# Kernel optimization log

Measured on AMD Instinct MI355X. Metric: run time of the kernel, lower is better.

Reference implementation:

```python
import jax, jax.numpy as jnp
import numpy as np

N = 50000
E = 800000
F_IN = 256
C = 64  # embedding_size, heads=1
EDGE_DIM = 2
NEG_SLOPE = 0.01


def setup_inputs() -> dict:
    key = jax.random.key(0)
    ks = jax.random.split(key, 12)
    s = 1.0 / np.sqrt(C)
    return {
        "x": jax.random.normal(ks[0], (N, F_IN), jnp.float32),
        "edge_index": jax.random.randint(ks[1], (2, E), 0, N, jnp.int64),
        "edge_attr": jax.random.normal(ks[2], (E, EDGE_DIM), jnp.float32),
        "Wf": jax.random.normal(ks[3], (F_IN, C), jnp.float32) / np.sqrt(F_IN),
        "bf": jnp.zeros((C,), jnp.float32),
        "Wq": jax.random.normal(ks[4], (C, C), jnp.float32) * s,
        "bq": jnp.zeros((C,), jnp.float32),
        "Wk": jax.random.normal(ks[5], (C, C), jnp.float32) * s,
        "bk": jnp.zeros((C,), jnp.float32),
        "Wv": jax.random.normal(ks[6], (C, C), jnp.float32) * s,
        "bv": jnp.zeros((C,), jnp.float32),
        "We": jax.random.normal(ks[7], (EDGE_DIM, C), jnp.float32) / np.sqrt(EDGE_DIM),
        "Wskip": jax.random.normal(ks[8], (C, C), jnp.float32) * s,
        "bskip": jnp.zeros((C,), jnp.float32),
    }


def reference(x, edge_index, edge_attr, Wf, bf, Wq, bq, Wk, bk, Wv, bv, We, Wskip, bskip):
    n = x.shape[0]
    src, dst = edge_index[0], edge_index[1]
    inv_sqrt_c = 1.0 / np.sqrt(C)

    h = jax.nn.leaky_relu(x @ Wf + bf, NEG_SLOPE)
    e = edge_attr @ We  # [E, C] edge embedding (lin_edge, no bias), same each layer

    for _ in range(3):
        q = h @ Wq + bq
        k = h @ Wk + bk
        v = h @ Wv + bv
        kj = k[src] + e                                  # [E, C] key + edge feat
        alpha = jnp.sum(q[dst] * kj, axis=-1) * inv_sqrt_c  # [E]
        # per-destination softmax
        m = jax.ops.segment_max(alpha, dst, num_segments=n)
        ex = jnp.exp(alpha - m[dst])
        den = jax.ops.segment_sum(ex, dst, num_segments=n)
        a = ex / den[dst]                                # [E]
        msg = (v[src] + e) * a[:, None]                  # [E, C]
        agg = jax.ops.segment_sum(msg, dst, num_segments=n)  # [N, C]
        h = jax.nn.leaky_relu(agg + h @ Wskip + bskip, NEG_SLOPE)  # root_weight skip
    return h
```

## Files before the change

### kernel.cpp

```cpp
#include <hip/hip_runtime.h>
#include <hip/hip_fp16.h>

#define NN 50000
#define NE 800000
#define FIN 256
#define C 64
#define NEG_SLOPE 0.01f
#define SCAN_BLOCKS ((NN + 255) / 256)
#define CSR_CHUNKS (NE / 256)

typedef float f32x16 __attribute__((ext_vector_type(16)));

__device__ __forceinline__ float leaky(float v) { return v > 0.f ? v : NEG_SLOPE * v; }

__global__ __launch_bounds__(256) void k_tw(const float* __restrict__ Wq,
                                            const float* __restrict__ Wk,
                                            const float* __restrict__ Wv,
                                            const float* __restrict__ Ws,
                                            float* __restrict__ Wt) {
    const int idx = blockIdx.x * 256 + threadIdx.x;
    if (idx >= 4 * 64 * 64) return;
    const int m = idx >> 12, r = idx & 4095, c = r >> 6, k = r & 63;
    const float* W = (m == 0) ? Wq : (m == 1) ? Wk : (m == 2) ? Wv : Ws;
    Wt[idx] = W[k * 64 + c];
}

#define FEAT_NPB 16

__global__ __launch_bounds__(256) void k_feat(const float* __restrict__ x,
                                              const float* __restrict__ Wf,
                                              const float* __restrict__ bf,
                                              float* __restrict__ h) {
    __shared__ float4 Sx[FEAT_NPB][64];
    __shared__ float part[FEAT_NPB][4][64];
    const int t = threadIdx.x;
    const int lane = t & 63;
    const int w = __builtin_amdgcn_readfirstlane(t) >> 6;
    const int base = blockIdx.x * FEAT_NPB;

    const float4* x4 = (const float4*)x;
#pragma unroll
    for (int i = 0; i < 4; ++i) {
        const int idx = t + i * 256;
        const int row = idx >> 6, c4 = idx & 63;
        Sx[row][c4] = x4[(size_t)(base + row) * 64 + c4];
    }

    float wrk[64];
#pragma unroll
    for (int k = 0; k < 64; ++k)
        wrk[k] = Wf[(size_t)(w * 64 + k) * 64 + lane];

    __syncthreads();

#pragma unroll
    for (int i = 0; i < FEAT_NPB; ++i) {
        float a0 = 0.f, a1 = 0.f, a2 = 0.f, a3 = 0.f;
#pragma unroll
        for (int j = 0; j < 16; ++j) {
            const float4 xv = Sx[i][w * 16 + j];
            a0 = fmaf(xv.x, wrk[4 * j + 0], a0);
            a1 = fmaf(xv.y, wrk[4 * j + 1], a1);
            a2 = fmaf(xv.z, wrk[4 * j + 2], a2);
            a3 = fmaf(xv.w, wrk[4 * j + 3], a3);
        }
        part[i][w][lane] = (a0 + a1) + (a2 + a3);
    }
    __syncthreads();

#pragma unroll
    for (int j = 0; j < 4; ++j) {
        const int o = t + j * 256;
        const int node = o >> 6, col = o & 63;
        const float r = part[node][0][col] + part[node][1][col]
                      + part[node][2][col] + part[node][3][col] + bf[col];
        h[(size_t)(base + node) * 64 + col] = leaky(r);
    }
}

#define QKVS_NPB 32

__global__ __launch_bounds__(256) void k_qkvs(const float* __restrict__ h,
                                              const float* __restrict__ Wt,
                                              const float* __restrict__ bq,
                                              const float* __restrict__ bk,
                                              const float* __restrict__ bv,
                                              const float* __restrict__ bs,
                                              float* __restrict__ qkvs) {
    const int t = threadIdx.x;
    const int lane = t & 63;
    const int sec = __builtin_amdgcn_readfirstlane(t) >> 6;
    const int base = blockIdx.x * QKVS_NPB;

    int m, cidx;
    float bias;
    if (sec == 0)      { m = 0; cidx = lane; bias = bq[lane]; }
    else if (sec == 1) { m = 3; cidx = lane; bias = bs[lane]; }
    else {
        cidx = ((sec - 2) << 5) + (lane >> 1);
        m = 1 + (lane & 1);
        bias = (lane & 1) ? bv[cidx] : bk[cidx];
    }

    const float4* wb = (const float4*)(Wt + ((size_t)m << 12) + ((size_t)cidx << 6));
    float4 w[16];
#pragma unroll
    for (int j = 0; j < 16; ++j) w[j] = wb[j];

    const int nmax = (base + QKVS_NPB <= NN) ? QKVS_NPB : (NN - base);
    for (int i = 0; i < nmax; ++i) {
        const float* hrow = h + (size_t)(base + i) * 64;
        f32x16 ha, hb, hc, hd;
        asm volatile("s_load_dwordx16 %0, %4, 0x0\n\t"
                     "s_load_dwordx16 %1, %4, 0x40\n\t"
                     "s_load_dwordx16 %2, %4, 0x80\n\t"
                     "s_load_dwordx16 %3, %4, 0xc0\n\t"
                     "s_waitcnt lgkmcnt(0)"
                     : "=&s"(ha), "=&s"(hb), "=&s"(hc), "=&s"(hd)
                     : "s"(hrow));
        float a0 = 0.f, a1 = 0.f, a2 = 0.f, a3 = 0.f;
#pragma unroll
        for (int j = 0; j < 4; ++j) {
            a0 = fmaf(ha[4 * j + 0], w[j].x, a0);
            a1 = fmaf(ha[4 * j + 1], w[j].y, a1);
            a2 = fmaf(ha[4 * j + 2], w[j].z, a2);
            a3 = fmaf(ha[4 * j + 3], w[j].w, a3);
        }
#pragma unroll
        for (int j = 0; j < 4; ++j) {
            a0 = fmaf(hb[4 * j + 0], w[4 + j].x, a0);
            a1 = fmaf(hb[4 * j + 1], w[4 + j].y, a1);
            a2 = fmaf(hb[4 * j + 2], w[4 + j].z, a2);
            a3 = fmaf(hb[4 * j + 3], w[4 + j].w, a3);
        }
#pragma unroll
        for (int j = 0; j < 4; ++j) {
            a0 = fmaf(hc[4 * j + 0], w[8 + j].x, a0);
            a1 = fmaf(hc[4 * j + 1], w[8 + j].y, a1);
            a2 = fmaf(hc[4 * j + 2], w[8 + j].z, a2);
            a3 = fmaf(hc[4 * j + 3], w[8 + j].w, a3);
        }
#pragma unroll
        for (int j = 0; j < 4; ++j) {
            a0 = fmaf(hd[4 * j + 0], w[12 + j].x, a0);
            a1 = fmaf(hd[4 * j + 1], w[12 + j].y, a1);
            a2 = fmaf(hd[4 * j + 2], w[12 + j].z, a2);
            a3 = fmaf(hd[4 * j + 3], w[12 + j].w, a3);
        }
        const float val = ((a0 + a1) + (a2 + a3)) + bias;
        float* orow = qkvs + (size_t)(base + i) * 192;
        if (sec == 0) {
            orow[lane] = val;
        } else if (sec == 1) {
            orow[128 + lane] = val;
        } else {
            __half* kvh = (__half*)(orow + 64);
            kvh[((sec - 2) << 6) + lane] = __float2half(val);
        }
    }
}

__global__ __launch_bounds__(256) void k_hist(const int* __restrict__ ei,
                                              int* __restrict__ deg) {
    const int e = blockIdx.x * 256 + threadIdx.x;
    if (e >= NE) return;
    atomicAdd(&deg[ei[NE + e]], 1);
}

__global__ __launch_bounds__(256) void k_blocksum(const int* __restrict__ deg,
                                                  int* __restrict__ bsum) {
    __shared__ int sh[256];
    const int t = threadIdx.x;
    const int idx = blockIdx.x * 256 + t;
    sh[t] = (idx < NN) ? deg[idx] : 0;
    __syncthreads();
#pragma unroll
    for (int off = 128; off > 0; off >>= 1) {
        if (t < off) sh[t] += sh[t + off];
        __syncthreads();
    }
    if (t == 0) bsum[blockIdx.x] = sh[0];
}

__global__ __launch_bounds__(256) void k_scanb(const int* __restrict__ bsum,
                                               int* __restrict__ boff) {
    __shared__ int sh[256];
    const int t = threadIdx.x;
    const int v = (t < SCAN_BLOCKS) ? bsum[t] : 0;
    sh[t] = v;
    __syncthreads();
#pragma unroll
    for (int off = 1; off < 256; off <<= 1) {
        const int x = (t >= off) ? sh[t - off] : 0;
        __syncthreads();
        sh[t] += x;
        __syncthreads();
    }
    if (t < SCAN_BLOCKS) boff[t] = sh[t] - v;
}

__global__ __launch_bounds__(256) void k_writeptr(const int* __restrict__ deg,
                                                  const int* __restrict__ boff,
                                                  int* __restrict__ row_ptr,
                                                  int* __restrict__ cursor) {
    __shared__ int sh[256];
    const int t = threadIdx.x;
    const int idx = blockIdx.x * 256 + t;
    const int v = (idx < NN) ? deg[idx] : 0;
    sh[t] = v;
    __syncthreads();
#pragma unroll
    for (int off = 1; off < 256; off <<= 1) {
        const int x = (t >= off) ? sh[t - off] : 0;
        __syncthreads();
        sh[t] += x;
        __syncthreads();
    }
    if (idx < NN) {
        const int r = boff[blockIdx.x] + sh[t] - v;
        row_ptr[idx] = r;
        cursor[idx] = r;
    }
    if (idx == 0) row_ptr[NN] = NE;
}

__global__ __launch_bounds__(256) void k_csr(const int* __restrict__ ei,
                                             const float* __restrict__ eattr,
                                             const int* __restrict__ row_ptr,
                                             int* __restrict__ cursor,
                                             uint2* __restrict__ erec) {
    const int chunk = blockIdx.x >> 3;
    const unsigned myx = blockIdx.x & 7;
    const int e = chunk * 256 + threadIdx.x;
    const int dst = ei[NE + e];
    const int rp = row_ptr[dst];
    const unsigned owner = (unsigned)rp / (NE / 8u);
    if (owner != myx) return;
    const int pos = atomicAdd(&cursor[dst], 1);
    const __half2 a = __floats2half2_rn(eattr[e * 2], eattr[e * 2 + 1]);
    erec[pos] = make_uint2((unsigned)ei[e], *(const unsigned*)&a);
}

__global__ __launch_bounds__(256) void k_conv(const int* __restrict__ row_ptr,
                                              const uint2* __restrict__ erec,
                                              const float* __restrict__ We,
                                              const float* __restrict__ qkvs,
                                              float* __restrict__ hout) {
    const int t = threadIdx.x;
    const int lane = t & 63;
    const int g = lane >> 4;
    const int p = lane & 15;
    const int wv = __builtin_amdgcn_readfirstlane(t) >> 6;
    const int d = blockIdx.x * 4 + wv;
    if (d >= NN) return;

    const float* qrow = qkvs + (size_t)d * 192;
    const float4 q4  = *(const float4*)(qrow + 4 * p);
    const float4 w0  = *(const float4*)(We + 4 * p);
    const float4 w1  = *(const float4*)(We + 64 + 4 * p);

    float pg0 = q4.x * w0.x + q4.y * w0.y + q4.z * w0.z + q4.w * w0.w;
    float pg1 = q4.x * w1.x + q4.y * w1.y + q4.z * w1.z + q4.w * w1.w;
#pragma unroll
    for (int mask = 1; mask <= 8; mask <<= 1) {
        pg0 += __shfl_xor(pg0, mask);
        pg1 += __shfl_xor(pg1, mask);
    }
    const float g0 = pg0, g1 = pg1;

    const int i0 = row_ptr[d], i1 = row_ptr[d + 1];
    const char* kvbase = (const char*)qkvs + 256 + ((size_t)p << 4);

    float m = -1e30f, l = 0.f, S1 = 0.f, S2 = 0.f;
    float4 acc = make_float4(0.f, 0.f, 0.f, 0.f);

#pragma unroll 2
    for (int i = i0 + g; i < i1; i += 4) {
        const uint2 r = erec[i];
        const __half2 ah = *(const __half2*)&r.y;
        const float a0 = __low2float(ah), a1 = __high2float(ah);
        const float4 kvl = *(const float4*)(kvbase + (size_t)r.x * 768);
        const __half2* hv = (const __half2*)&kvl;
        const float kf0 = __low2float(hv[0]), vf0 = __high2float(hv[0]);
        const float kf1 = __low2float(hv[1]), vf1 = __high2float(hv[1]);
        const float kf2 = __low2float(hv[2]), vf2 = __high2float(hv[2]);
        const float kf3 = __low2float(hv[3]), vf3 = __high2float(hv[3]);
        float dot = q4.x * kf0 + q4.y * kf1 + q4.z * kf2 + q4.w * kf3;
        dot += __shfl_xor(dot, 1);
        dot += __shfl_xor(dot, 2);
        dot += __shfl_xor(dot, 4);
        dot += __shfl_xor(dot, 8);
        const float P = (dot + g0 * a0 + g1 * a1) * 0.125f;
        const float mn = fmaxf(m, P);
        const float s = __expf(m - mn);
        const float e = __expf(P - mn);
        l = l * s + e;
        acc.x = acc.x * s + vf0 * e;
        acc.y = acc.y * s + vf1 * e;
        acc.z = acc.z * s + vf2 * e;
        acc.w = acc.w * s + vf3 * e;
        S1 = S1 * s + a0 * e;
        S2 = S2 * s + a1 * e;
        m = mn;
    }

#pragma unroll
    for (int mask = 16; mask <= 32; mask <<= 1) {
        const float mo  = __shfl_xor(m, mask);
        const float lo  = __shfl_xor(l, mask);
        const float axo = __shfl_xor(acc.x, mask);
        const float ayo = __shfl_xor(acc.y, mask);
        const float azo = __shfl_xor(acc.z, mask);
        const float awo = __shfl_xor(acc.w, mask);
        const float S1o = __shfl_xor(S1, mask);
        const float S2o = __shfl_xor(S2, mask);
        const float mn = fmaxf(m, mo);
        const float sA = __expf(m - mn);
        const float sB = __expf(mo - mn);
        l     = l * sA + lo * sB;
        acc.x = acc.x * sA + axo * sB;
        acc.y = acc.y * sA + ayo * sB;
        acc.z = acc.z * sA + azo * sB;
        acc.w = acc.w * sA + awo * sB;
        S1    = S1 * sA + S1o * sB;
        S2    = S2 * sA + S2o * sB;
        m = mn;
    }

    if (lane < 16) {
        const float inv = (l > 0.f) ? 1.f / l : 0.f;
        const float4 sk = *(const float4*)(qrow + 128 + 4 * p);
        float4 r;
        r.x = leaky((acc.x + S1 * w0.x + S2 * w1.x) * inv + sk.x);
        r.y = leaky((acc.y + S1 * w0.y + S2 * w1.y) * inv + sk.y);
        r.z = leaky((acc.z + S1 * w0.z + S2 * w1.z) * inv + sk.z);
        r.w = leaky((acc.w + S1 * w0.w + S2 * w1.w) * inv + sk.w);
        *(float4*)(hout + (size_t)d * C + 4 * p) = r;
    }
}

extern "C" void kernel_launch(void* const* d_in, const int* in_sizes, int n_in,
                              void* d_out, int out_size, void* d_ws, size_t ws_size,
                              hipStream_t stream) {
    const float* x     = (const float*)d_in[0];
    const int*   ei    = (const int*)d_in[1];
    const float* eattr = (const float*)d_in[2];
    const float* Wf    = (const float*)d_in[3];
    const float* bf    = (const float*)d_in[4];
    const float* Wq    = (const float*)d_in[5];
    const float* bq    = (const float*)d_in[6];
    const float* Wk    = (const float*)d_in[7];
    const float* bk    = (const float*)d_in[8];
    const float* Wv    = (const float*)d_in[9];
    const float* bv    = (const float*)d_in[10];
    const float* We    = (const float*)d_in[11];
    const float* Ws    = (const float*)d_in[12];
    const float* bs    = (const float*)d_in[13];
    float* out = (float*)d_out;

    char* p = (char*)d_ws;
    float*  h       = (float*)p;  p += (size_t)NN * C * 4;
    float*  qkvs    = (float*)p;  p += (size_t)NN * 192 * 4;
    float*  Wt      = (float*)p;  p += (size_t)4 * 64 * 64 * 4;
    int*    deg     = (int*)p;    p += (size_t)NN * 4;
    int*    row_ptr = (int*)p;    p += (size_t)(NN + 1) * 4;
    int*    cursor  = (int*)p;    p += (size_t)NN * 4;
    int*    bsum    = (int*)p;    p += (size_t)SCAN_BLOCKS * 4;
    int*    boff    = (int*)p;    p += (size_t)SCAN_BLOCKS * 4;
    uint2*  erec    = (uint2*)p;  p += (size_t)NE * 8;

    k_tw<<<64, 256, 0, stream>>>(Wq, Wk, Wv, Ws, Wt);
    hipMemsetAsync(deg, 0, (size_t)NN * 4, stream);
    k_hist<<<CSR_CHUNKS, 256, 0, stream>>>(ei, deg);
    k_blocksum<<<SCAN_BLOCKS, 256, 0, stream>>>(deg, bsum);
    k_scanb<<<1, 256, 0, stream>>>(bsum, boff);
    k_writeptr<<<SCAN_BLOCKS, 256, 0, stream>>>(deg, boff, row_ptr, cursor);
    k_csr<<<CSR_CHUNKS * 8, 256, 0, stream>>>(ei, eattr, row_ptr, cursor, erec);

    const int feat_grid = NN / FEAT_NPB;
    const int qkvs_grid = (NN + QKVS_NPB - 1) / QKVS_NPB;

    k_feat<<<feat_grid, 256, 0, stream>>>(x, Wf, bf, h);

    for (int layer = 0; layer < 3; ++layer) {
        k_qkvs<<<qkvs_grid, 256, 0, stream>>>(h, Wt, bq, bk, bv, bs, qkvs);
        float* hout = (layer == 2) ? out : h;
        k_conv<<<(NN + 3) / 4, 256, 0, stream>>>(row_ptr, erec, We, qkvs, hout);
    }
}
```

Baseline: 488.9 us.

## Restructure input feature GEMM with per-lane node rows and scalar-loaded weights

Rewrites the x@Wf kernel so each block handles 64 nodes, with each lane owning one node and each wave owning 16 output columns. Weights are fetched as wave-uniform values through inline s_load_dwordx16 into scalar registers, and x is staged in padded shared memory in two K-phases. This removes the cross-wave partial-sum reduction and the per-thread 64-register weight preload, and raises reuse of x per block. In exchange it issues a blocking scalar-memory wait on every K step and needs an extra LDS pass to coalesce the output stores.

```diff
diff --git a/kernel.cpp b/kernel.cpp
--- a/kernel.cpp
+++ b/kernel.cpp
@@ -25,56 +25,88 @@
     Wt[idx] = W[k * 64 + c];
 }
 
-#define FEAT_NPB 16
-
 __global__ __launch_bounds__(256) void k_feat(const float* __restrict__ x,
                                               const float* __restrict__ Wf,
                                               const float* __restrict__ bf,
                                               float* __restrict__ h) {
-    __shared__ float4 Sx[FEAT_NPB][64];
-    __shared__ float part[FEAT_NPB][4][64];
+    __shared__ float4 Sx[64][33];
     const int t = threadIdx.x;
     const int lane = t & 63;
-    const int w = __builtin_amdgcn_readfirstlane(t) >> 6;
-    const int base = blockIdx.x * FEAT_NPB;
+    const int q = __builtin_amdgcn_readfirstlane(t) >> 6;
+    const int base = blockIdx.x * 64;
 
     const float4* x4 = (const float4*)x;
+    float4 acc[4];
+#pragma unroll
+    for (int cp = 0; cp < 4; ++cp) acc[cp] = make_float4(0.f, 0.f, 0.f, 0.f);
+
+#define FRAG(wreg, xs)                                                      \
+    acc[0].x = fmaf(xs, wreg[0],  acc[0].x);                                \
+    acc[0].y = fmaf(xs, wreg[1],  acc[0].y);                                \
+    acc[0].z = fmaf(xs, wreg[2],  acc[0].z);                                \
+    acc[0].w = fmaf(xs, wreg[3],  acc[0].w);                                \
+    acc[1].x = fmaf(xs, wreg[4],  acc[1].x);                                \
+    acc[1].y = fmaf(xs, wreg[5],  acc[1].y);                                \
+    acc[1].z = fmaf(xs, wreg[6],  acc[1].z);                                \
+    acc[1].w = fmaf(xs, wreg[7],  acc[1].w);                                \
+    acc[2].x = fmaf(xs, wreg[8],  acc[2].x);                                \
+    acc[2].y = fmaf(xs, wreg[9],  acc[2].y);                                \
+    acc[2].z = fmaf(xs, wreg[10], acc[2].z);                                \
+    acc[2].w = fmaf(xs, wreg[11], acc[2].w);                                \
+    acc[3].x = fmaf(xs, wreg[12], acc[3].x);                                \
+    acc[3].y = fmaf(xs, wreg[13], acc[3].y);                                \
+    acc[3].z = fmaf(xs, wreg[14], acc[3].z);                                \
+    acc[3].w = fmaf(xs, wreg[15], acc[3].w);
+
+    for (int ph = 0; ph < 2; ++ph) {
+#pragma unroll
+        for (int i = 0; i < 8; ++i) {
+            const int idx = t + i * 256;
+            const int row = idx >> 5, c = idx & 31;
+            int nn = base + row; if (nn >= NN) nn = NN - 1;
+            Sx[row][c] = x4[(size_t)nn * 64 + ph * 32 + c];
+        }
+        __syncthreads();
+
+        const float* wbase = Wf + (size_t)(ph * 128) * 64 + q * 16;
+#pragma unroll
+        for (int j = 0; j < 32; ++j) {
+            const float4 xv = Sx[lane][j];
+            const float* wrow = wbase + (size_t)j * 256;
+            f32x16 w0_, w1_, w2_, w3_;
+            asm volatile("s_load_dwordx16 %0, %4, 0x0\n\t"
+                         "s_load_dwordx16 %1, %4, 0x100\n\t"
+                         "s_load_dwordx16 %2, %4, 0x200\n\t"
+                         "s_load_dwordx16 %3, %4, 0x300\n\t"
+                         "s_waitcnt lgkmcnt(0)"
+                         : "=&s"(w0_), "=&s"(w1_), "=&s"(w2_), "=&s"(w3_)
+                         : "s"(wrow));
+            FRAG(w0_, xv.x)
+            FRAG(w1_, xv.y)
+            FRAG(w2_, xv.z)
+            FRAG(w3_, xv.w)
+        }
+        __syncthreads();
+    }
+#undef FRAG
+
+    float4* O = (float4*)Sx;
+    const float4* bf4 = (const float4*)bf;
+#pragma unroll
+    for (int cp = 0; cp < 4; ++cp) {
+        const float4 b = bf4[q * 4 + cp];
+        float4 r;
+        r.x = leaky(acc[cp].x + b.x); r.y = leaky(acc[cp].y + b.y);
+        r.z = leaky(acc[cp].z + b.z); r.w = leaky(acc[cp].w + b.w);
+        O[lane * 17 + q * 4 + cp] = r;
+    }
+    __syncthreads();
 #pragma unroll
     for (int i = 0; i < 4; ++i) {
         const int idx = t + i * 256;
-        const int row = idx >> 6, c4 = idx & 63;
-        Sx[row][c4] = x4[(size_t)(base + row) * 64 + c4];
-    }
-
-    float wrk[64];
-#pragma unroll
-    for (int k = 0; k < 64; ++k)
-        wrk[k] = Wf[(size_t)(w * 64 + k) * 64 + lane];
-
-    __syncthreads();
-
-#pragma unroll
-    for (int i = 0; i < FEAT_NPB; ++i) {
-        float a0 = 0.f, a1 = 0.f, a2 = 0.f, a3 = 0.f;
-#pragma unroll
-        for (int j = 0; j < 16; ++j) {
-            const float4 xv = Sx[i][w * 16 + j];
-            a0 = fmaf(xv.x, wrk[4 * j + 0], a0);
-            a1 = fmaf(xv.y, wrk[4 * j + 1], a1);
-            a2 = fmaf(xv.z, wrk[4 * j + 2], a2);
-            a3 = fmaf(xv.w, wrk[4 * j + 3], a3);
-        }
-        part[i][w][lane] = (a0 + a1) + (a2 + a3);
-    }
-    __syncthreads();
-
-#pragma unroll
-    for (int j = 0; j < 4; ++j) {
-        const int o = t + j * 256;
-        const int node = o >> 6, col = o & 63;
-        const float r = part[node][0][col] + part[node][1][col]
-                      + part[node][2][col] + part[node][3][col] + bf[col];
-        h[(size_t)(base + node) * 64 + col] = leaky(r);
+        const int row = idx >> 4, c = idx & 15;
+        const int nn = base + row;
+        if (nn < NN) ((float4*)h)[(size_t)nn * 16 + c] = O[row * 17 + c];
     }
 }
 
@@ -377,7 +409,7 @@
     k_writeptr<<<SCAN_BLOCKS, 256, 0, stream>>>(deg, boff, row_ptr, cursor);
     k_csr<<<CSR_CHUNKS * 8, 256, 0, stream>>>(ei, eattr, row_ptr, cursor, erec);
 
-    const int feat_grid = NN / FEAT_NPB;
+    const int feat_grid = (NN + 63) / 64;
     const int qkvs_grid = (NN + QKVS_NPB - 1) / QKVS_NPB;
 
     k_feat<<<feat_grid, 256, 0, stream>>>(x, Wf, bf, h);
```

Result: no change. 482.6 us (-1.3%).
